# Performance work log

Hardware: AMD Instinct MI355X
Metric: run time of the kernel (lower is better)

Reference implementation:

```python
import jax, jax.numpy as jnp
import numpy as np

B, H, L = 32768, 512, 10          # batch, hidden_dim, act_max_layer
THRESHOLD = 0.9                    # 1 - act_epsilon
EPS = 1e-15


def setup_inputs() -> dict:
    key = jax.random.key(0)
    ks = jax.random.split(key, 8)
    s = 1.0 / np.sqrt(H)
    return {
        "inputs": jax.random.normal(ks[0], (B, H), jnp.float32),
        "hidden": jax.random.normal(ks[1], (B, H), jnp.float32),
        # halting MLP: Linear(H,H) -> ReLU -> (Dropout, identity in eval) -> Linear(H,1) -> Sigmoid
        "halt_w1": jax.random.uniform(ks[2], (H, H), jnp.float32, -s, s),
        "halt_b1": jnp.zeros((H,), jnp.float32),
        "halt_w2": jax.random.uniform(ks[3], (1, H), jnp.float32, -s, s),
        "halt_b2": jnp.zeros((1,), jnp.float32),
        # torch.nn.GRUCell parameters, gate row order [r; z; n]
        "w_ih": jax.random.uniform(ks[4], (3 * H, H), jnp.float32, -s, s),
        "w_hh": jax.random.uniform(ks[5], (3 * H, H), jnp.float32, -s, s),
        "b_ih": jnp.zeros((3 * H,), jnp.float32),
        "b_hh": jnp.zeros((3 * H,), jnp.float32),
        # learnt depth embedding (act_max_layer, hidden_dim)
        "depth_emb": 0.02 * jax.random.normal(ks[6], (L, H), jnp.float32),
    }


def _gru_cell(x, h, w_ih, w_hh, b_ih, b_hh):
    gi = x @ w_ih.T + b_ih            # (B, 3H)
    gh = h @ w_hh.T + b_hh            # (B, 3H)
    i_r, i_z, i_n = jnp.split(gi, 3, axis=-1)
    h_r, h_z, h_n = jnp.split(gh, 3, axis=-1)
    r = jax.nn.sigmoid(i_r + h_r)
    z = jax.nn.sigmoid(i_z + h_z)
    n = jnp.tanh(i_n + r * h_n)
    return (1.0 - z) * n + z * h


def reference(inputs, hidden, halt_w1, halt_b1, halt_w2, halt_b2,
              w_ih, w_hh, b_ih, b_hh, depth_emb):
    def step(carry, emb):
        h, cum = carry
        alive = (cum < 1.0).astype(jnp.float32)                       # (B,)
        p = jax.nn.sigmoid(
            jax.nn.relu(h @ halt_w1.T + halt_b1) @ halt_w2.T + halt_b2
        )[:, 0]                                                        # (B,)
        new_halted = (p * alive + cum > THRESHOLD).astype(jnp.float32)
        remainder = 1.0 - cum + EPS
        alive = (1.0 - new_halted) * alive
        p_step = p * alive + remainder * new_halted
        cum = cum + p_step
        # attention-None quirk: step input is the hidden state (+ depth emb),
        # the original `inputs` tensor is never fed to the RNN cell.
        x = h + emb[None, :]
        h_new = _gru_cell(x, h, w_ih, w_hh, b_ih, b_hh)
        return (h_new, cum), (h, alive, p_step)

    cum0 = jnp.zeros((inputs.shape[0],), jnp.float32)
    (_, _), (hs, alives, psteps) = jax.lax.scan(step, (hidden, cum0), depth_emb)
    # hs: (L, B, H); alives, psteps: (L, B)
    merged = jnp.einsum("lbh,lb->bh", hs, psteps)      # MEAN_FIELD merge
    accumulated_halting = jnp.sum(psteps * alives, axis=0)  # (B,)
    num_updated = jnp.sum(alives, axis=0)                   # (B,)
    return merged, accumulated_halting, num_updated
```

## Files before the change

kernel.cpp:

```cpp
#include <hip/hip_runtime.h>


typedef __attribute__((ext_vector_type(8))) short bf16x8;
typedef __attribute__((ext_vector_type(4))) float f32x4;

#define BM 128

__device__ __forceinline__ unsigned short f2bf(float x) {
    unsigned int u = __float_as_uint(x);
    u += 0x7fffu + ((u >> 16) & 1u);
    return (unsigned short)(u >> 16);
}
__device__ __forceinline__ float bf2f(unsigned short b) {
    return __uint_as_float(((unsigned int)b) << 16);
}
__device__ __forceinline__ int swz(int r, int kc) { return kc ^ ((r ^ (r >> 2)) & 3); }

__global__ void k_init(float* __restrict__ cum, int* __restrict__ idxA,
                       int* __restrict__ counts, int B) {
    int i = blockIdx.x * blockDim.x + threadIdx.x;
    if (i < B) { cum[i] = 0.f; idxA[i] = i; }
    if (i == 0) { counts[0] = B; for (int l = 1; l < 16; ++l) counts[l] = 0; }
}

__global__ void k_split(const float* __restrict__ x, unsigned short* __restrict__ hi,
                        unsigned short* __restrict__ lo, int n8) {
    int i = blockIdx.x * blockDim.x + threadIdx.x;
    if (i >= n8) return;
    const float4 v0 = ((const float4*)x)[2 * i];
    const float4 v1 = ((const float4*)x)[2 * i + 1];
    float v[8] = {v0.x, v0.y, v0.z, v0.w, v1.x, v1.y, v1.z, v1.w};
    bf16x8 vh, vl;
    #pragma unroll
    for (int e = 0; e < 8; ++e) {
        unsigned short h = f2bf(v[e]);
        vh[e] = (short)h;
        vl[e] = (short)f2bf(v[e] - bf2f(h));
    }
    *(bf16x8*)&hi[(long long)i * 8] = vh;
    *(bf16x8*)&lo[(long long)i * 8] = vl;
}

__global__ void k_prep_w1f(const float* __restrict__ w1, unsigned short* __restrict__ fhi,
                           unsigned short* __restrict__ flo) {
    int i = blockIdx.x * blockDim.x + threadIdx.x;
    if (i >= 4 * 16 * 8 * 64 * 8) return;
    int e = i & 7, l = (i >> 3) & 63, j = (i >> 9) & 7, ks = (i >> 12) & 15, ct = i >> 16;
    int col = ct * 128 + j * 16 + (l & 15);
    int k = ks * 32 + (l >> 4) * 8 + e;
    float v = w1[(long long)col * 512 + k];
    unsigned short h = f2bf(v);
    fhi[i] = h;
    flo[i] = f2bf(v - bf2f(h));
}

__global__ void k_prep_wgf(const float* __restrict__ w_ih, const float* __restrict__ w_hh,
                           unsigned short* __restrict__ fhi, unsigned short* __restrict__ flo) {
    int i = blockIdx.x * blockDim.x + threadIdx.x;
    if (i >= 32 * 16 * 6 * 64 * 8) return;
    int e = i & 7, l = (i >> 3) & 63;
    int t = i >> 9;
    int j = t % 6;
    int ksct = t / 6;
    int ks = ksct & 15, ct = ksct >> 4;
    int col = ct * 96 + j * 16 + (l & 15);
    int u = col / 6, g = col % 6;
    int k = ks * 32 + (l >> 4) * 8 + e;
    float v = (g < 3) ? w_ih[((long long)(g * 512 + u)) * 512 + k]
                      : w_hh[((long long)((g - 3) * 512 + u)) * 512 + k];
    unsigned short h = f2bf(v);
    fhi[i] = h;
    flo[i] = f2bf(v - bf2f(h));
}

__global__ void k_prep_cg(const float* __restrict__ emb, const float* __restrict__ w_ih,
                          const float* __restrict__ b_ih, const float* __restrict__ b_hh,
                          float* __restrict__ cg, int L) {
    int total = L * 6 * 512;
    for (int i = blockIdx.x * blockDim.x + threadIdx.x; i < total;
         i += gridDim.x * blockDim.x) {
        int g = i % 6;
        int u = (i / 6) % 512;
        int l = i / (6 * 512);
        float v;
        if (g < 3) {
            const float* w = w_ih + (long long)(g * 512 + u) * 512;
            const float* e = emb + (long long)l * 512;
            float s = 0.f;
            #pragma unroll 8
            for (int k = 0; k < 512; ++k) s = fmaf(e[k], w[k], s);
            v = s + b_ih[g * 512 + u];
        } else {
            v = b_hh[(g - 3) * 512 + u];
        }
        cg[i] = v;
    }
}

__global__ __launch_bounds__(256) void k_halt(
        const unsigned short* __restrict__ hhi, const unsigned short* __restrict__ hlo,
        const int* __restrict__ idx, const int* __restrict__ counts, int lslot,
        const unsigned short* __restrict__ w1hi, const unsigned short* __restrict__ w1lo,
        const float* __restrict__ b1, const float* __restrict__ w2,
        float* __restrict__ p_part) {
    int n = counts[lslot];
    int rt = blockIdx.x, ct = blockIdx.y;
    if (rt * BM >= n) return;
    __shared__ unsigned short sA[2 * 4096];
    __shared__ int rid[BM];
    int tid = threadIdx.x;
    if (tid < BM) rid[tid] = idx[min(rt * BM + tid, n - 1)];
    __syncthreads();
    int w = tid >> 6, l = tid & 63;
    f32x4 acc[2][8];
    #pragma unroll
    for (int a = 0; a < 2; ++a)
        #pragma unroll
        for (int j = 0; j < 8; ++j) acc[a][j] = (f32x4){0.f, 0.f, 0.f, 0.f};

    for (int ks = 0; ks < 16; ++ks) {
        int k0 = ks * 32;
        #pragma unroll
        for (int q = 0; q < 4; ++q) {
            int c = tid + q * 256;
            int s = c >> 9, r = (c >> 2) & 127, kc = c & 3;
            const unsigned short* src = (s ? hlo : hhi) + (long long)rid[r] * 512 + k0 + kc * 8;
            bf16x8 v = *(const bf16x8*)src;
            *(bf16x8*)&sA[s * 4096 + r * 32 + 8 * swz(r, kc)] = v;
        }
        __syncthreads();
        bf16x8 ahi[2], alo[2];
        #pragma unroll
        for (int a = 0; a < 2; ++a) {
            int r = w * 32 + a * 16 + (l & 15);
            int off = r * 32 + 8 * swz(r, l >> 4);
            ahi[a] = *(const bf16x8*)&sA[off];
            alo[a] = *(const bf16x8*)&sA[4096 + off];
        }
        #pragma unroll
        for (int j = 0; j < 8; ++j) {
            int fb = ((((ct * 16 + ks) * 8 + j) * 64) + l) * 8;
            bf16x8 bh = *(const bf16x8*)&w1hi[fb];
            bf16x8 bl = *(const bf16x8*)&w1lo[fb];
            #pragma unroll
            for (int a = 0; a < 2; ++a) {
                acc[a][j] = __builtin_amdgcn_mfma_f32_16x16x32_bf16(ahi[a], bh, acc[a][j], 0, 0, 0);
                acc[a][j] = __builtin_amdgcn_mfma_f32_16x16x32_bf16(alo[a], bh, acc[a][j], 0, 0, 0);
                acc[a][j] = __builtin_amdgcn_mfma_f32_16x16x32_bf16(ahi[a], bl, acc[a][j], 0, 0, 0);
            }
        }
        __syncthreads();
    }
    int q = l >> 4;
    float sums[2][4];
    #pragma unroll
    for (int a = 0; a < 2; ++a)
        #pragma unroll
        for (int r = 0; r < 4; ++r) sums[a][r] = 0.f;
    #pragma unroll
    for (int j = 0; j < 8; ++j) {
        int cb = ct * 128 + j * 16 + (l & 15);
        float bb = b1[cb], ww = w2[cb];
        #pragma unroll
        for (int a = 0; a < 2; ++a)
            #pragma unroll
            for (int r = 0; r < 4; ++r) {
                float v = acc[a][j][r] + bb;
                v = v > 0.f ? v : 0.f;
                sums[a][r] = fmaf(v, ww, sums[a][r]);
            }
    }
    #pragma unroll
    for (int m = 1; m < 16; m <<= 1)
        #pragma unroll
        for (int a = 0; a < 2; ++a)
            #pragma unroll
            for (int r = 0; r < 4; ++r) sums[a][r] += __shfl_xor(sums[a][r], m, 64);
    if ((l & 15) == 0) {
        #pragma unroll
        for (int a = 0; a < 2; ++a)
            #pragma unroll
            for (int r = 0; r < 4; ++r) {
                int pos = rt * BM + w * 32 + a * 16 + q * 4 + r;
                if (pos < n) p_part[(long long)pos * 4 + ct] = sums[a][r];
            }
    }
}

__global__ void k_book(const float* __restrict__ p_part, const float* __restrict__ b2,
                       float* __restrict__ cum,
                       const unsigned short* __restrict__ hhi,
                       const unsigned short* __restrict__ hlo,
                       const int* __restrict__ idx, const int* __restrict__ counts, int lslot,
                       float* __restrict__ out, int* __restrict__ idx_next,
                       int* __restrict__ count_next, int B, int first) {
    int n = counts[lslot];
    int wv = (blockIdx.x * blockDim.x + threadIdx.x) >> 6;
    int lane = threadIdx.x & 63;
    int nw = (gridDim.x * blockDim.x) >> 6;
    for (int pos = wv; pos < n; pos += nw) {
        int row = idx[pos];
        float ps = 0.f;
        if (lane == 0) {
            float s = p_part[(long long)pos * 4 + 0] + p_part[(long long)pos * 4 + 1] +
                      p_part[(long long)pos * 4 + 2] + p_part[(long long)pos * 4 + 3] + b2[0];
            float p = 1.f / (1.f + expf(-s));
            float cb = cum[row];
            int halted = (p + cb > 0.9f);
            float rem = (1.f - cb) + 1e-15f;
            ps = halted ? rem : p;
            cum[row] = cb + ps;
            long long BH = (long long)B * 512;
            if (first) {
                out[BH + row]     = halted ? 0.f : ps;
                out[BH + B + row] = halted ? 0.f : 1.f;
            } else if (!halted) {
                out[BH + row]     += ps;
                out[BH + B + row] += 1.f;
            }
            if (!halted) idx_next[atomicAdd(count_next, 1)] = row;
        }
        ps = __shfl(ps, 0, 64);
        long long hb = (long long)row * 512 + lane * 8;
        bf16x8 vh = *(const bf16x8*)&hhi[hb];
        bf16x8 vl = *(const bf16x8*)&hlo[hb];
        float* mr = out + hb;
        float vals[8];
        #pragma unroll
        for (int e = 0; e < 8; ++e)
            vals[e] = bf2f((unsigned short)vh[e]) + bf2f((unsigned short)vl[e]);
        if (first) {
            #pragma unroll
            for (int e = 0; e < 8; ++e) mr[e] = vals[e] * ps;
        } else {
            #pragma unroll
            for (int e = 0; e < 8; ++e) mr[e] = fmaf(vals[e], ps, mr[e]);
        }
    }
}

__global__ __launch_bounds__(256) void k_gru(
        const unsigned short* __restrict__ hhi, const unsigned short* __restrict__ hlo,
        const int* __restrict__ idx, const int* __restrict__ counts, int lslot,
        const unsigned short* __restrict__ wghi, const unsigned short* __restrict__ wglo,
        const float* __restrict__ cgl,
        unsigned short* __restrict__ nhi, unsigned short* __restrict__ nlo) {
    int n = counts[lslot];
    int rt = blockIdx.x, ct = blockIdx.y;
    if (rt * BM >= n) return;
    __shared__ unsigned int smem[12416];
    __shared__ int rid[BM];
    unsigned short* sA = (unsigned short*)smem;
    float* gt = (float*)smem;
    int tid = threadIdx.x;
    if (tid < BM) rid[tid] = idx[min(rt * BM + tid, n - 1)];
    __syncthreads();
    int w = tid >> 6, l = tid & 63;
    f32x4 acc[2][6];
    #pragma unroll
    for (int a = 0; a < 2; ++a)
        #pragma unroll
        for (int j = 0; j < 6; ++j) acc[a][j] = (f32x4){0.f, 0.f, 0.f, 0.f};

    for (int ks = 0; ks < 16; ++ks) {
        int k0 = ks * 32;
        #pragma unroll
        for (int q = 0; q < 4; ++q) {
            int c = tid + q * 256;
            int s = c >> 9, r = (c >> 2) & 127, kc = c & 3;
            const unsigned short* src = (s ? hlo : hhi) + (long long)rid[r] * 512 + k0 + kc * 8;
            bf16x8 v = *(const bf16x8*)src;
            *(bf16x8*)&sA[s * 4096 + r * 32 + 8 * swz(r, kc)] = v;
        }
        __syncthreads();
        bf16x8 ahi[2], alo[2];
        #pragma unroll
        for (int a = 0; a < 2; ++a) {
            int r = w * 32 + a * 16 + (l & 15);
            int off = r * 32 + 8 * swz(r, l >> 4);
            ahi[a] = *(const bf16x8*)&sA[off];
            alo[a] = *(const bf16x8*)&sA[4096 + off];
        }
        #pragma unroll
        for (int j = 0; j < 6; ++j) {
            int fb = ((((ct * 16 + ks) * 6 + j) * 64) + l) * 8;
            bf16x8 bh = *(const bf16x8*)&wghi[fb];
            bf16x8 bl = *(const bf16x8*)&wglo[fb];
            #pragma unroll
            for (int a = 0; a < 2; ++a) {
                acc[a][j] = __builtin_amdgcn_mfma_f32_16x16x32_bf16(ahi[a], bh, acc[a][j], 0, 0, 0);
                acc[a][j] = __builtin_amdgcn_mfma_f32_16x16x32_bf16(alo[a], bh, acc[a][j], 0, 0, 0);
                acc[a][j] = __builtin_amdgcn_mfma_f32_16x16x32_bf16(ahi[a], bl, acc[a][j], 0, 0, 0);
            }
        }
        __syncthreads();
    }
    int q = l >> 4;
    #pragma unroll
    for (int a = 0; a < 2; ++a)
        #pragma unroll
        for (int j = 0; j < 6; ++j)
            #pragma unroll
            for (int r = 0; r < 4; ++r)
                gt[(w * 32 + a * 16 + q * 4 + r) * 97 + j * 16 + (l & 15)] = acc[a][j][r];
    __syncthreads();
    int row = tid >> 1, ub = (tid & 1) * 8;
    int pos = rt * BM + row;
    if (pos < n) {
        int grow = rid[row];
        bf16x8 vh, vl;
        #pragma unroll
        for (int ui = 0; ui < 8; ++ui) {
            int u = ub + ui;
            const float* g = &gt[row * 97 + u * 6];
            int ug = ct * 16 + u;
            const float* c6 = &cgl[ug * 6];
            float ir = g[0] + c6[0], iz = g[1] + c6[1], in_ = g[2] + c6[2];
            float hr = g[3] + c6[3], hz = g[4] + c6[4], hn = g[5] + c6[5];
            float r = 1.f / (1.f + expf(-(ir + hr)));
            float z = 1.f / (1.f + expf(-(iz + hz)));
            float nn = tanhf(fmaf(r, hn, in_));
            long long off = (long long)grow * 512 + ug;
            float ho = bf2f(hhi[off]) + bf2f(hlo[off]);
            float hv = (1.f - z) * nn + z * ho;
            unsigned short hb = f2bf(hv);
            vh[ui] = (short)hb;
            vl[ui] = (short)f2bf(hv - bf2f(hb));
        }
        long long ob = (long long)grow * 512 + ct * 16 + ub;
        *(bf16x8*)&nhi[ob] = vh;
        *(bf16x8*)&nlo[ob] = vl;
    }
}

extern "C" void kernel_launch(void* const* d_in, const int* in_sizes, int n_in,
                              void* d_out, int out_size, void* d_ws, size_t ws_size,
                              hipStream_t stream) {
    const float* hidden  = (const float*)d_in[1];
    const float* halt_w1 = (const float*)d_in[2];
    const float* halt_b1 = (const float*)d_in[3];
    const float* halt_w2 = (const float*)d_in[4];
    const float* halt_b2 = (const float*)d_in[5];
    const float* w_ih    = (const float*)d_in[6];
    const float* w_hh    = (const float*)d_in[7];
    const float* b_ih    = (const float*)d_in[8];
    const float* b_hh    = (const float*)d_in[9];
    const float* demb    = (const float*)d_in[10];

    const int H = in_sizes[3];
    const int B = in_sizes[1] / H;
    const int L = in_sizes[10] / H;

    float* out = (float*)d_out;

    char* wsp = (char*)d_ws;
    auto alloc = [&](size_t bytes) {
        char* p = wsp;
        wsp += (bytes + 255) & ~(size_t)255;
        return p;
    };
    unsigned short* hAhi = (unsigned short*)alloc((size_t)B * 512 * 2);
    unsigned short* hAlo = (unsigned short*)alloc((size_t)B * 512 * 2);
    unsigned short* hBhi = (unsigned short*)alloc((size_t)B * 512 * 2);
    unsigned short* hBlo = (unsigned short*)alloc((size_t)B * 512 * 2);
    unsigned short* w1fh = (unsigned short*)alloc((size_t)262144 * 2);
    unsigned short* w1fl = (unsigned short*)alloc((size_t)262144 * 2);
    unsigned short* wgfh = (unsigned short*)alloc((size_t)1572864 * 2);
    unsigned short* wgfl = (unsigned short*)alloc((size_t)1572864 * 2);
    float* cg    = (float*)alloc((size_t)L * 6 * 512 * 4);
    float* ppart = (float*)alloc((size_t)B * 4 * 4);
    float* cum   = (float*)alloc((size_t)B * 4);
    int* idxA    = (int*)alloc((size_t)B * 4);
    int* idxB    = (int*)alloc((size_t)B * 4);
    int* counts  = (int*)alloc(64);
    (void)ws_size; (void)n_in; (void)out_size;

    k_init<<<(B + 255) / 256, 256, 0, stream>>>(cum, idxA, counts, B);
    k_split<<<(B * 512 / 8 + 255) / 256, 256, 0, stream>>>(hidden, hAhi, hAlo, B * 512 / 8);
    k_prep_w1f<<<1024, 256, 0, stream>>>(halt_w1, w1fh, w1fl);
    k_prep_wgf<<<6144, 256, 0, stream>>>(w_ih, w_hh, wgfh, wgfl);
    k_prep_cg<<<120, 256, 0, stream>>>(demb, w_ih, b_ih, b_hh, cg, L);

    unsigned short* hch = hAhi; unsigned short* hcl = hAlo;
    unsigned short* hnh = hBhi; unsigned short* hnl = hBlo;
    int* ia = idxA;
    int* ib = idxB;

    dim3 hgrid((B + BM - 1) / BM, 4);
    dim3 ggrid((B + BM - 1) / BM, 32);

    for (int l = 0; l < L; ++l) {
        k_halt<<<hgrid, 256, 0, stream>>>(hch, hcl, ia, counts, l, w1fh, w1fl,
                                          halt_b1, halt_w2, ppart);
        k_book<<<8192, 256, 0, stream>>>(ppart, halt_b2, cum, hch, hcl, ia, counts, l,
                                         out, ib, counts + (l + 1), B, l == 0 ? 1 : 0);
        if (l + 1 < L) {
            k_gru<<<ggrid, 256, 0, stream>>>(hch, hcl, ib, counts, l + 1, wgfh, wgfl,
                                             cg + (size_t)l * 6 * 512, hnh, hnl);
            unsigned short* t;
            t = hch; hch = hnh; hnh = t;
            t = hcl; hcl = hnl; hnl = t;
            int* ti = ia; ia = ib; ib = ti;
        }
    }
}
```

Measured before the change: 1.764 ms.

## Load MFMA A fragments directly from global and compute GRU gates in registers

The halt and GRU GEMM kernels drop the shared-memory staging of the gathered hidden rows. Each lane now loads its A fragments straight from global memory, which removes two barriers per k-step. The GRU weight fragments are re-laid out so that the six gates of one hidden unit share a lane column, letting the gate nonlinearity run directly on the accumulators. Shared memory then only holds a small old-hidden and output tile instead of a 97-wide gate tile. Launch bounds now request 3 blocks per CU. The trade-off is redundant global loads of A across column tiles with no LDS reuse, plus register pressure from the occupancy hint.

```diff
diff --git a/kernel.cpp b/kernel.cpp
--- a/kernel.cpp
+++ b/kernel.cpp
@@ -14,7 +14,6 @@
 __device__ __forceinline__ float bf2f(unsigned short b) {
     return __uint_as_float(((unsigned int)b) << 16);
 }
-__device__ __forceinline__ int swz(int r, int kc) { return kc ^ ((r ^ (r >> 2)) & 3); }
 
 __global__ void k_init(float* __restrict__ cum, int* __restrict__ idxA,
                        int* __restrict__ counts, int B) {
@@ -60,14 +59,13 @@
     if (i >= 32 * 16 * 6 * 64 * 8) return;
     int e = i & 7, l = (i >> 3) & 63;
     int t = i >> 9;
-    int j = t % 6;
+    int g = t % 6;
     int ksct = t / 6;
     int ks = ksct & 15, ct = ksct >> 4;
-    int col = ct * 96 + j * 16 + (l & 15);
-    int u = col / 6, g = col % 6;
+    int unit = ct * 16 + (l & 15);
     int k = ks * 32 + (l >> 4) * 8 + e;
-    float v = (g < 3) ? w_ih[((long long)(g * 512 + u)) * 512 + k]
-                      : w_hh[((long long)((g - 3) * 512 + u)) * 512 + k];
+    float v = (g < 3) ? w_ih[((long long)(g * 512 + unit)) * 512 + k]
+                      : w_hh[((long long)((g - 3) * 512 + unit)) * 512 + k];
     unsigned short h = f2bf(v);
     fhi[i] = h;
     flo[i] = f2bf(v - bf2f(h));
@@ -97,7 +95,7 @@
     }
 }
 
-__global__ __launch_bounds__(256) void k_halt(
+__global__ __launch_bounds__(256, 3) void k_halt(
         const unsigned short* __restrict__ hhi, const unsigned short* __restrict__ hlo,
         const int* __restrict__ idx, const int* __restrict__ counts, int lslot,
         const unsigned short* __restrict__ w1hi, const unsigned short* __restrict__ w1lo,
@@ -106,12 +104,19 @@
     int n = counts[lslot];
     int rt = blockIdx.x, ct = blockIdx.y;
     if (rt * BM >= n) return;
-    __shared__ unsigned short sA[2 * 4096];
-    __shared__ int rid[BM];
     int tid = threadIdx.x;
-    if (tid < BM) rid[tid] = idx[min(rt * BM + tid, n - 1)];
-    __syncthreads();
     int w = tid >> 6, l = tid & 63;
+    int p0 = rt * BM + w * 32 + (l & 15);
+    int r0 = idx[min(p0, n - 1)];
+    int r1 = idx[min(p0 + 16, n - 1)];
+    int ko = (l >> 4) * 8;
+    const unsigned short* a0h = hhi + (long long)r0 * 512 + ko;
+    const unsigned short* a0l = hlo + (long long)r0 * 512 + ko;
+    const unsigned short* a1h = hhi + (long long)r1 * 512 + ko;
+    const unsigned short* a1l = hlo + (long long)r1 * 512 + ko;
+    const unsigned short* pbh = w1hi + (long long)ct * 65536 + l * 8;
+    const unsigned short* pbl = w1lo + (long long)ct * 65536 + l * 8;
+
     f32x4 acc[2][8];
     #pragma unroll
     for (int a = 0; a < 2; ++a)
@@ -119,37 +124,21 @@
         for (int j = 0; j < 8; ++j) acc[a][j] = (f32x4){0.f, 0.f, 0.f, 0.f};
 
     for (int ks = 0; ks < 16; ++ks) {
-        int k0 = ks * 32;
-        #pragma unroll
-        for (int q = 0; q < 4; ++q) {
-            int c = tid + q * 256;
-            int s = c >> 9, r = (c >> 2) & 127, kc = c & 3;
-            const unsigned short* src = (s ? hlo : hhi) + (long long)rid[r] * 512 + k0 + kc * 8;
-            bf16x8 v = *(const bf16x8*)src;
-            *(bf16x8*)&sA[s * 4096 + r * 32 + 8 * swz(r, kc)] = v;
-        }
-        __syncthreads();
-        bf16x8 ahi[2], alo[2];
-        #pragma unroll
-        for (int a = 0; a < 2; ++a) {
-            int r = w * 32 + a * 16 + (l & 15);
-            int off = r * 32 + 8 * swz(r, l >> 4);
-            ahi[a] = *(const bf16x8*)&sA[off];
-            alo[a] = *(const bf16x8*)&sA[4096 + off];
-        }
+        bf16x8 va0h = *(const bf16x8*)(a0h + ks * 32);
+        bf16x8 va0l = *(const bf16x8*)(a0l + ks * 32);
+        bf16x8 va1h = *(const bf16x8*)(a1h + ks * 32);
+        bf16x8 va1l = *(const bf16x8*)(a1l + ks * 32);
         #pragma unroll
         for (int j = 0; j < 8; ++j) {
-            int fb = ((((ct * 16 + ks) * 8 + j) * 64) + l) * 8;
-            bf16x8 bh = *(const bf16x8*)&w1hi[fb];
-            bf16x8 bl = *(const bf16x8*)&w1lo[fb];
-            #pragma unroll
-            for (int a = 0; a < 2; ++a) {
-                acc[a][j] = __builtin_amdgcn_mfma_f32_16x16x32_bf16(ahi[a], bh, acc[a][j], 0, 0, 0);
-                acc[a][j] = __builtin_amdgcn_mfma_f32_16x16x32_bf16(alo[a], bh, acc[a][j], 0, 0, 0);
-                acc[a][j] = __builtin_amdgcn_mfma_f32_16x16x32_bf16(ahi[a], bl, acc[a][j], 0, 0, 0);
-            }
-        }
-        __syncthreads();
+            bf16x8 bh = *(const bf16x8*)(pbh + ks * 4096 + j * 512);
+            bf16x8 bl = *(const bf16x8*)(pbl + ks * 4096 + j * 512);
+            acc[0][j] = __builtin_amdgcn_mfma_f32_16x16x32_bf16(va0h, bh, acc[0][j], 0, 0, 0);
+            acc[0][j] = __builtin_amdgcn_mfma_f32_16x16x32_bf16(va0l, bh, acc[0][j], 0, 0, 0);
+            acc[0][j] = __builtin_amdgcn_mfma_f32_16x16x32_bf16(va0h, bl, acc[0][j], 0, 0, 0);
+            acc[1][j] = __builtin_amdgcn_mfma_f32_16x16x32_bf16(va1h, bh, acc[1][j], 0, 0, 0);
+            acc[1][j] = __builtin_amdgcn_mfma_f32_16x16x32_bf16(va1l, bh, acc[1][j], 0, 0, 0);
+            acc[1][j] = __builtin_amdgcn_mfma_f32_16x16x32_bf16(va1h, bl, acc[1][j], 0, 0, 0);
+        }
     }
     int q = l >> 4;
     float sums[2][4];
@@ -239,7 +228,7 @@
     }
 }
 
-__global__ __launch_bounds__(256) void k_gru(
+__global__ __launch_bounds__(256, 3) void k_gru(
         const unsigned short* __restrict__ hhi, const unsigned short* __restrict__ hlo,
         const int* __restrict__ idx, const int* __restrict__ counts, int lslot,
         const unsigned short* __restrict__ wghi, const unsigned short* __restrict__ wglo,
@@ -248,88 +237,89 @@
     int n = counts[lslot];
     int rt = blockIdx.x, ct = blockIdx.y;
     if (rt * BM >= n) return;
-    __shared__ unsigned int smem[12416];
-    __shared__ int rid[BM];
-    unsigned short* sA = (unsigned short*)smem;
-    float* gt = (float*)smem;
+    __shared__ float hx[128 * 20];
     int tid = threadIdx.x;
-    if (tid < BM) rid[tid] = idx[min(rt * BM + tid, n - 1)];
+    int w = tid >> 6, l = tid & 63;
+    int p0 = rt * BM + w * 32 + (l & 15);
+    int r0 = idx[min(p0, n - 1)];
+    int r1 = idx[min(p0 + 16, n - 1)];
+    int ko = (l >> 4) * 8;
+    const unsigned short* a0h = hhi + (long long)r0 * 512 + ko;
+    const unsigned short* a0l = hlo + (long long)r0 * 512 + ko;
+    const unsigned short* a1h = hhi + (long long)r1 * 512 + ko;
+    const unsigned short* a1l = hlo + (long long)r1 * 512 + ko;
+    const unsigned short* pbh = wghi + (long long)ct * 49152 + l * 8;
+    const unsigned short* pbl = wglo + (long long)ct * 49152 + l * 8;
+    int ug = ct * 16 + (l & 15);
+    float cgv[6];
+    #pragma unroll
+    for (int g = 0; g < 6; ++g) cgv[g] = cgl[ug * 6 + g];
+
+    f32x4 acc[2][6];
+    #pragma unroll
+    for (int a = 0; a < 2; ++a)
+        #pragma unroll
+        for (int g = 0; g < 6; ++g) acc[a][g] = (f32x4){0.f, 0.f, 0.f, 0.f};
+
+    for (int ks = 0; ks < 16; ++ks) {
+        bf16x8 va0h = *(const bf16x8*)(a0h + ks * 32);
+        bf16x8 va0l = *(const bf16x8*)(a0l + ks * 32);
+        bf16x8 va1h = *(const bf16x8*)(a1h + ks * 32);
+        bf16x8 va1l = *(const bf16x8*)(a1l + ks * 32);
+        #pragma unroll
+        for (int g = 0; g < 6; ++g) {
+            bf16x8 bh = *(const bf16x8*)(pbh + ks * 3072 + g * 512);
+            bf16x8 bl = *(const bf16x8*)(pbl + ks * 3072 + g * 512);
+            acc[0][g] = __builtin_amdgcn_mfma_f32_16x16x32_bf16(va0h, bh, acc[0][g], 0, 0, 0);
+            acc[0][g] = __builtin_amdgcn_mfma_f32_16x16x32_bf16(va0l, bh, acc[0][g], 0, 0, 0);
+            acc[0][g] = __builtin_amdgcn_mfma_f32_16x16x32_bf16(va0h, bl, acc[0][g], 0, 0, 0);
+            acc[1][g] = __builtin_amdgcn_mfma_f32_16x16x32_bf16(va1h, bh, acc[1][g], 0, 0, 0);
+            acc[1][g] = __builtin_amdgcn_mfma_f32_16x16x32_bf16(va1l, bh, acc[1][g], 0, 0, 0);
+            acc[1][g] = __builtin_amdgcn_mfma_f32_16x16x32_bf16(va1h, bl, acc[1][g], 0, 0, 0);
+        }
+    }
+
+    int erow = tid >> 1, eub = (tid & 1) * 8;
+    int epos = rt * BM + erow;
+    int egrow = idx[min(epos, n - 1)];
+    long long hb = (long long)egrow * 512 + ct * 16 + eub;
+    {
+        bf16x8 oh = *(const bf16x8*)&hhi[hb];
+        bf16x8 ol = *(const bf16x8*)&hlo[hb];
+        #pragma unroll
+        for (int e = 0; e < 8; ++e)
+            hx[erow * 20 + eub + e] = bf2f((unsigned short)oh[e]) + bf2f((unsigned short)ol[e]);
+    }
     __syncthreads();
-    int w = tid >> 6, l = tid & 63;
-    f32x4 acc[2][6];
     #pragma unroll
     for (int a = 0; a < 2; ++a)
         #pragma unroll
-        for (int j = 0; j < 6; ++j) acc[a][j] = (f32x4){0.f, 0.f, 0.f, 0.f};
-
-    for (int ks = 0; ks < 16; ++ks) {
-        int k0 = ks * 32;
-        #pragma unroll
-        for (int q = 0; q < 4; ++q) {
-            int c = tid + q * 256;
-            int s = c >> 9, r = (c >> 2) & 127, kc = c & 3;
-            const unsigned short* src = (s ? hlo : hhi) + (long long)rid[r] * 512 + k0 + kc * 8;
-            bf16x8 v = *(const bf16x8*)src;
-            *(bf16x8*)&sA[s * 4096 + r * 32 + 8 * swz(r, kc)] = v;
-        }
-        __syncthreads();
-        bf16x8 ahi[2], alo[2];
-        #pragma unroll
-        for (int a = 0; a < 2; ++a) {
-            int r = w * 32 + a * 16 + (l & 15);
-            int off = r * 32 + 8 * swz(r, l >> 4);
-            ahi[a] = *(const bf16x8*)&sA[off];
-            alo[a] = *(const bf16x8*)&sA[4096 + off];
-        }
-        #pragma unroll
-        for (int j = 0; j < 6; ++j) {
-            int fb = ((((ct * 16 + ks) * 6 + j) * 64) + l) * 8;
-            bf16x8 bh = *(const bf16x8*)&wghi[fb];
-            bf16x8 bl = *(const bf16x8*)&wglo[fb];
-            #pragma unroll
-            for (int a = 0; a < 2; ++a) {
-                acc[a][j] = __builtin_amdgcn_mfma_f32_16x16x32_bf16(ahi[a], bh, acc[a][j], 0, 0, 0);
-                acc[a][j] = __builtin_amdgcn_mfma_f32_16x16x32_bf16(alo[a], bh, acc[a][j], 0, 0, 0);
-                acc[a][j] = __builtin_amdgcn_mfma_f32_16x16x32_bf16(ahi[a], bl, acc[a][j], 0, 0, 0);
-            }
-        }
-        __syncthreads();
-    }
-    int q = l >> 4;
-    #pragma unroll
-    for (int a = 0; a < 2; ++a)
-        #pragma unroll
-        for (int j = 0; j < 6; ++j)
-            #pragma unroll
-            for (int r = 0; r < 4; ++r)
-                gt[(w * 32 + a * 16 + q * 4 + r) * 97 + j * 16 + (l & 15)] = acc[a][j][r];
+        for (int r = 0; r < 4; ++r) {
+            int row = w * 32 + a * 16 + (l >> 4) * 4 + r;
+            float ho = hx[row * 20 + (l & 15)];
+            float ir  = acc[a][0][r] + cgv[0];
+            float iz  = acc[a][1][r] + cgv[1];
+            float in_ = acc[a][2][r] + cgv[2];
+            float hr  = acc[a][3][r] + cgv[3];
+            float hz  = acc[a][4][r] + cgv[4];
+            float hn  = acc[a][5][r] + cgv[5];
+            float rr = 1.f / (1.f + expf(-(ir + hr)));
+            float z  = 1.f / (1.f + expf(-(iz + hz)));
+            float nn = tanhf(fmaf(rr, hn, in_));
+            hx[row * 20 + (l & 15)] = (1.f - z) * nn + z * ho;
+        }
     __syncthreads();
-    int row = tid >> 1, ub = (tid & 1) * 8;
-    int pos = rt * BM + row;
-    if (pos < n) {
-        int grow = rid[row];
+    if (epos < n) {
         bf16x8 vh, vl;
         #pragma unroll
-        for (int ui = 0; ui < 8; ++ui) {
-            int u = ub + ui;
-            const float* g = &gt[row * 97 + u * 6];
-            int ug = ct * 16 + u;
-            const float* c6 = &cgl[ug * 6];
-            float ir = g[0] + c6[0], iz = g[1] + c6[1], in_ = g[2] + c6[2];
-            float hr = g[3] + c6[3], hz = g[4] + c6[4], hn = g[5] + c6[5];
-            float r = 1.f / (1.f + expf(-(ir + hr)));
-            float z = 1.f / (1.f + expf(-(iz + hz)));
-            float nn = tanhf(fmaf(r, hn, in_));
-            long long off = (long long)grow * 512 + ug;
-            float ho = bf2f(hhi[off]) + bf2f(hlo[off]);
-            float hv = (1.f - z) * nn + z * ho;
-            unsigned short hb = f2bf(hv);
-            vh[ui] = (short)hb;
-            vl[ui] = (short)f2bf(hv - bf2f(hb));
-        }
-        long long ob = (long long)grow * 512 + ct * 16 + ub;
-        *(bf16x8*)&nhi[ob] = vh;
-        *(bf16x8*)&nlo[ob] = vl;
+        for (int e = 0; e < 8; ++e) {
+            float v = hx[erow * 20 + eub + e];
+            unsigned short hbv = f2bf(v);
+            vh[e] = (short)hbv;
+            vl[e] = (short)f2bf(v - bf2f(hbv));
+        }
+        *(bf16x8*)&nhi[hb] = vh;
+        *(bf16x8*)&nlo[hb] = vl;
     }
 }
 
```

Measured after the change: 1.541 ms. 12.6% less time.
